# Kernel tuning notes

Hardware: AMD Instinct MI355X
Metric: run time of the kernel (lower is better)

Reference implementation:

```python
import jax, jax.numpy as jnp
import numpy as np

N, E, EL = 50000, 150000, 300000   # atoms, bonds(=line-graph nodes), line-graph edges
FN, FE, FX = 128, 128, 64          # atom, bond, angle feature dims (encode_dim)
H, D = 4, 64                        # num_heads, per-head hidden
SLOPE = 0.01                        # torch leaky_relu default


def _leaky(x):
    return jnp.where(x >= 0, x, SLOPE * x)


def _seg_softmax(logits, seg, n):
    # softmax over edges grouped by destination (DGL edge_softmax). logits [E, H]
    m = jax.ops.segment_max(logits, seg, num_segments=n)
    ex = jnp.exp(logits - m[seg])
    s = jax.ops.segment_sum(ex, seg, num_segments=n)
    return ex / s[seg]


def _seg_mean(x, seg, n):
    # mean of incoming edge feats per dst node; empty segments -> 0 (DGL behavior)
    s = jax.ops.segment_sum(x, seg, num_segments=n)
    c = jax.ops.segment_sum(jnp.ones((x.shape[0], 1), x.dtype), seg, num_segments=n)
    return s / jnp.maximum(c, 1.0)


def setup_inputs() -> dict:
    key = jax.random.key(0)
    ks = iter(jax.random.split(key, 40))
    nrm = lambda shape, sc=0.1: jax.random.normal(next(ks), shape, jnp.float32) * sc
    z = lambda n: jnp.zeros((n,), jnp.float32)
    inp = {
        'nfeats': nrm((N, FN), 1.0),
        'efeats': nrm((E, FE), 1.0),
        'xfeats': nrm((EL, FX), 1.0),
        # EGAT layer (atom graph)
        'e_Wni': nrm((H * D, FN)), 'e_Wnj': nrm((H * D, FN)), 'e_Wfij': nrm((H * D, FE)),
        'e_Wnode': nrm((H * D, FN + FE)), 'e_bnode': z(H * D),
        'e_attn': nrm((H, D)), 'e_bias': z(H * D),
        # Path_Complex line-graph branch
        'lg_Wni': nrm((H * D, D)), 'lg_Wnj': nrm((H * D, D)), 'lg_Wfij': nrm((H * D, FX)),
        'lg_Wnode': nrm((H * D, D + FX)), 'lg_bnode': z(H * D),
        'lg_attn': nrm((H, D)), 'lg_bias': z(H * D),
        # Path_Complex graph branch
        'g_Wni': nrm((H * D, D)), 'g_Wnj': nrm((H * D, D)), 'g_Wfij': nrm((H * D, D)),
        'g_Wnode': nrm((H * D, D + D)), 'g_bnode': z(H * D),
        'g_attn': nrm((H, D)), 'g_bias': z(H * D),
        # graph / line-graph connectivity
        'src': jax.random.randint(next(ks), (E,), 0, N, jnp.int32),
        'dst': jax.random.randint(next(ks), (E,), 0, N, jnp.int32),
        'lsrc': jax.random.randint(next(ks), (EL,), 0, E, jnp.int32),
        'ldst': jax.random.randint(next(ks), (EL,), 0, E, jnp.int32),
    }
    return inp


def _forward(nfeats, efeats, xfeats,
             e_Wni, e_Wnj, e_Wfij, e_Wnode, e_bnode, e_attn, e_bias,
             lg_Wni, lg_Wnj, lg_Wfij, lg_Wnode, lg_bnode, lg_attn, lg_bias,
             g_Wni, g_Wnj, g_Wfij, g_Wnode, g_bnode, g_attn, g_bias,
             src, dst, lsrc, ldst):
    # ---- EGAT layer on atom graph ----
    fo = _leaky((nfeats @ e_Wni.T)[src] + (nfeats @ e_Wnj.T)[dst] + efeats @ e_Wfij.T + e_bias)
    fov = fo.reshape(E, H, D)
    e_att = _seg_softmax((fov * e_attn[None]).sum(-1), dst, N)      # [E, H]
    agg = _seg_mean(efeats, dst, N)                                   # [N, FE]
    h = (jnp.concatenate([nfeats, agg], 1) @ e_Wnode.T + e_bnode).reshape(N, H, D)
    h_node = _leaky(jax.ops.segment_sum(h[src] * e_att[:, :, None], dst, num_segments=N)).sum(1)
    f_edge = fov.sum(1)                                               # [E, D]

    # ---- Path_Complex layer: line-graph (bond->angle) branch ----
    lgf = _leaky((f_edge @ lg_Wni.T)[lsrc] + (f_edge @ lg_Wnj.T)[ldst] + xfeats @ lg_Wfij.T + lg_bias)
    lgv = lgf.reshape(EL, H, D)
    a_lg = _seg_softmax((lgv * lg_attn[None]).sum(-1), ldst, E)      # [EL, H]
    aggx = _seg_mean(xfeats, ldst, E)                                 # [E, FX]
    m1 = (jnp.concatenate([f_edge, aggx], 1) @ lg_Wnode.T + lg_bnode).reshape(E, H, D)
    lg_h = _leaky(jax.ops.segment_sum(m1[lsrc] * a_lg[:, :, None], ldst, num_segments=E)).sum(1)

    # ---- Path_Complex layer: graph (atom->bond) branch ----
    gf = _leaky((h_node @ g_Wni.T)[src] + (h_node @ g_Wnj.T)[dst] + f_edge @ g_Wfij.T + g_bias)
    gv = gf.reshape(E, H, D)
    a_g = _seg_softmax((gv * g_attn[None]).sum(-1), dst, N)          # [E, H] -> l_graph ndata 'a'
    node_edge = h_node[src] + h_node[dst]
    m2 = (jnp.concatenate([node_edge, f_edge], 1) @ g_Wnode.T + g_bnode).reshape(E, H, D)
    # u_mul_v on line graph: message = h_out[lsrc] * a[ldst]
    g_h = _leaky(jax.ops.segment_sum(m2[lsrc] * a_g[ldst][:, :, None], ldst, num_segments=E)).sum(1)

    return g_h + lg_h                                                 # [E, D] updated bond feats


def reference(nfeats, efeats, xfeats,
              e_Wni, e_Wnj, e_Wfij, e_Wnode, e_bnode, e_attn, e_bias,
              lg_Wni, lg_Wnj, lg_Wfij, lg_Wnode, lg_bnode, lg_attn, lg_bias,
              g_Wni, g_Wnj, g_Wfij, g_Wnode, g_bnode, g_attn, g_bias,
              src, dst, lsrc, ldst):
    return _forward(nfeats, efeats, xfeats,
                    e_Wni, e_Wnj, e_Wfij, e_Wnode, e_bnode, e_attn, e_bias,
                    lg_Wni, lg_Wnj, lg_Wfij, lg_Wnode, lg_bnode, lg_attn, lg_bias,
                    g_Wni, g_Wnj, g_Wfij, g_Wnode, g_bnode, g_attn, g_bias,
                    src, dst, lsrc, ldst)
```

## Files before the change

kernel.cpp:

```cpp
#include <hip/hip_runtime.h>
#include <hip/hip_bf16.h>
#include <math.h>

typedef __hip_bfloat16 bf16;
typedef short bf16x8 __attribute__((ext_vector_type(8)));
typedef short s16x4 __attribute__((ext_vector_type(4)));
typedef float f32x4 __attribute__((ext_vector_type(4)));

__device__ __forceinline__ float b2f(bf16 x) { return __bfloat162float(x); }
__device__ __forceinline__ bf16  f2b(float x) { return __float2bfloat16(x); }
__device__ __forceinline__ float leaky(float x) { return x >= 0.0f ? x : 0.01f * x; }
__device__ __forceinline__ float sb2f(short s) {
  return __uint_as_float(((unsigned)(unsigned short)s) << 16);
}
__device__ __forceinline__ short f2bs(float x) {
  unsigned u = __float_as_uint(x);
  u += 0x7FFFu + ((u >> 16) & 1u);
  return (short)(u >> 16);
}
__device__ __forceinline__ float ldF(const void* p, size_t i, int f) {
  return f ? ((const float*)p)[i] : b2f(((const bf16*)p)[i]);
}
__device__ __forceinline__ bf16x8 ldA8(const char* row, int k, int f) {
  if (!f) return *(const bf16x8*)(row + (size_t)k * 2);
  const float4* p = (const float4*)(row + (size_t)k * 4);
  float4 a = p[0], b = p[1];
  bf16x8 r;
  r[0] = f2bs(a.x); r[1] = f2bs(a.y); r[2] = f2bs(a.z); r[3] = f2bs(a.w);
  r[4] = f2bs(b.x); r[5] = f2bs(b.y); r[6] = f2bs(b.z); r[7] = f2bs(b.w);
  return r;
}
__device__ __forceinline__ bf16x8 ldA8sum(const bf16* base, int K0, int s, int t, int k) {
  bf16x8 u = *(const bf16x8*)(base + (size_t)s * K0 + k);
  bf16x8 v = *(const bf16x8*)(base + (size_t)t * K0 + k);
  bf16x8 r;
#pragma unroll
  for (int j = 0; j < 8; ++j) r[j] = f2bs(sb2f(u[j]) + sb2f(v[j]));
  return r;
}

__global__ void k_detect(const unsigned* __restrict__ w, int* __restrict__ flag) {
  __shared__ int cnt[256];
  unsigned x = w[threadIdx.x];
  unsigned ex = (x >> 7) & 0xFFu;
  cnt[threadIdx.x] = (ex >= 96u && ex <= 144u) ? 1 : 0;
  __syncthreads();
  for (int s = 128; s > 0; s >>= 1) {
    if (threadIdx.x < s) cnt[threadIdx.x] += cnt[threadIdx.x + s];
    __syncthreads();
  }
  if (threadIdx.x == 0) *flag = (cnt[0] < 128) ? 1 : 0;
}

struct WArgs { const void* src[21]; int beg[22]; int len[21]; };
__global__ void k_cvt_all(WArgs wa, bf16* __restrict__ dst, int total,
                          const int* __restrict__ flagp) {
  int f = *flagp;
  for (int i = blockIdx.x * 256 + threadIdx.x; i < total; i += gridDim.x * 256) {
    int t = 0;
    while (t < 20 && i >= wa.beg[t + 1]) ++t;
    int loc = i - wa.beg[t];
    bf16 v = f2b(0.0f);
    if (loc < wa.len[t])
      v = f ? f2b(((const float*)wa.src[t])[loc]) : ((const bf16*)wa.src[t])[loc];
    dst[i] = v;
  }
}

__global__ void k_cvt3(const float* __restrict__ a, bf16* __restrict__ da, size_t na,
                       const float* __restrict__ b, bf16* __restrict__ db, size_t nb,
                       const float* __restrict__ c, bf16* __restrict__ dc, size_t nc,
                       const int* __restrict__ flagp) {
  if (!*flagp) return;
  size_t tot = (na + nb + nc) >> 2;
  for (size_t i = (size_t)blockIdx.x * 256 + threadIdx.x; i < tot;
       i += (size_t)gridDim.x * 256) {
    size_t j = i << 2;
    const float* s; bf16* d; size_t loc;
    if (j < na)           { s = a; d = da; loc = j; }
    else if (j < na + nb) { s = b; d = db; loc = j - na; }
    else                  { s = c; d = dc; loc = j - na - nb; }
    float4 v = *(const float4*)(s + loc);
    s16x4 o; o[0] = f2bs(v.x); o[1] = f2bs(v.y); o[2] = f2bs(v.z); o[3] = f2bs(v.w);
    *(s16x4*)(d + loc) = o;
  }
}

__global__ void k_izero(int* __restrict__ p, int n) {
  int i = blockIdx.x * 256 + threadIdx.x;
  for (; i < n; i += gridDim.x * 256) p[i] = 0;
}

__global__ void k_hist(const int* __restrict__ seg, int* __restrict__ deg, int n) {
  int i = blockIdx.x * 256 + threadIdx.x;
  if (i < n) atomicAdd(&deg[seg[i]], 1);
}

__global__ __launch_bounds__(256)
void k_scan_local(const int* __restrict__ deg, int* __restrict__ rp,
                  int* __restrict__ bsum, int n) {
  __shared__ int sh[256];
  int tid = threadIdx.x;
  int base = blockIdx.x * 4096 + tid * 16;
  int v[16]; int s = 0;
#pragma unroll
  for (int j = 0; j < 16; ++j) { v[j] = (base + j < n) ? deg[base + j] : 0; s += v[j]; }
  sh[tid] = s;
  __syncthreads();
  for (int o = 1; o < 256; o <<= 1) {
    int t = (tid >= o) ? sh[tid - o] : 0;
    __syncthreads();
    sh[tid] += t;
    __syncthreads();
  }
  int run = sh[tid] - s;
#pragma unroll
  for (int j = 0; j < 16; ++j) {
    run += v[j];
    if (base + j < n) rp[base + j + 1] = run;
  }
  if (tid == 255) bsum[blockIdx.x] = sh[255];
  if (blockIdx.x == 0 && tid == 0) rp[0] = 0;
}
__global__ __launch_bounds__(256)
void k_scan_bsum(int* __restrict__ bsum, int nb) {
  __shared__ int sh[256];
  __shared__ int carry;
  int tid = threadIdx.x;
  if (tid == 0) carry = 0;
  __syncthreads();
  for (int base = 0; base < nb; base += 256) {
    int i = base + tid;
    int v = (i < nb) ? bsum[i] : 0;
    sh[tid] = v;
    __syncthreads();
    for (int o = 1; o < 256; o <<= 1) {
      int t = (tid >= o) ? sh[tid - o] : 0;
      __syncthreads();
      sh[tid] += t;
      __syncthreads();
    }
    if (i < nb) bsum[i] = carry + sh[tid] - v;
    int tot = sh[255];
    __syncthreads();
    if (tid == 0) carry += tot;
    __syncthreads();
  }
}
__global__ __launch_bounds__(256)
void k_scan_add(int* __restrict__ rp, const int* __restrict__ bsum, int n) {
  int b = blockIdx.x + 1;
  int ofs = bsum[b];
  int base = b * 4096 + threadIdx.x * 16;
#pragma unroll
  for (int j = 0; j < 16; ++j) {
    int idx = base + j + 1;
    if (idx <= n) rp[idx] += ofs;
  }
}

__global__ void k_slot(const int* __restrict__ seg, const int* __restrict__ rp,
                       int* __restrict__ cur, int* __restrict__ eid,
                       const int* __restrict__ aux, int* __restrict__ auxval,
                       int* __restrict__ pos, int n) {
  int i = blockIdx.x * 256 + threadIdx.x;
  if (i >= n) return;
  int t = seg[i];
  int p = atomicAdd(&cur[t], 1);
  int j = rp[t] + p;
  eid[j] = i;
  if (auxval) auxval[j] = aux[i];
  if (pos) pos[i] = j;
}

__global__ void k_gmean(const void* __restrict__ X, const void* __restrict__ Xc, int mode,
                        const int* __restrict__ rp, const int* __restrict__ eid,
                        bf16* __restrict__ out, int n, int width,
                        const int* __restrict__ flagp) {
  int f = (mode == 2) ? *flagp : mode;
  if (Xc && f) { X = Xc; f = 0; }
  int d = threadIdx.x;
  int row = blockIdx.x * blockDim.y + threadIdx.y;
  if (row >= n) return;
  int b = rp[row], e = rp[row + 1];
  float s = 0.0f;
  for (int j = b; j < e; ++j) s += ldF(X, (size_t)eid[j] * width + d, f);
  out[(size_t)row * width + d] = f2b(s / fmaxf((float)(e - b), 1.0f));
}

__global__ __launch_bounds__(256)
void k_mgemm(const void* __restrict__ A0, const void* __restrict__ A0c, int m0mode, int K0,
             const void* __restrict__ A1, int m1mode, int Ktot,
             const bf16* __restrict__ W, int whs, const bf16* __restrict__ bias,
             bf16* __restrict__ C, int cs, int M,
             const int* __restrict__ gs, const int* __restrict__ gd,
             const int* __restrict__ flagp) {
  int tid = threadIdx.x;
  int w = tid >> 6, lane = tid & 63, l15 = lane & 15, q = lane >> 4;
  int h = blockIdx.y;
  int fl = *flagp;
  int f0 = (m0mode == 2) ? fl : m0mode;
  if (A0c && f0) { A0 = A0c; f0 = 0; }
  int f1 = (m1mode == 2) ? fl : m1mode;
  const bf16* Wh = W + (size_t)h * whs;
  int colofs = h * 64;
  int m0 = blockIdx.x * 64 + w * 16;
  int mA = m0 + l15; if (mA > M - 1) mA = M - 1;
  int sA = 0, tA = 0;
  const char* rowA0 = nullptr;
  if (gs) { sA = gs[mA]; tA = gd[mA]; }
  else rowA0 = (const char*)A0 + (size_t)mA * K0 * (f0 ? 4 : 2);
  const char* rowA1 = A1 ? (const char*)A1 + (size_t)mA * (Ktot - K0) * (f1 ? 4 : 2) : nullptr;

  f32x4 acc[4] = {{0,0,0,0},{0,0,0,0},{0,0,0,0},{0,0,0,0}};
  for (int k = q * 8; k < Ktot; k += 32) {
    bf16x8 a;
    if (k < K0) a = gs ? ldA8sum((const bf16*)A0, K0, sA, tA, k) : ldA8(rowA0, k, f0);
    else        a = ldA8(rowA1, k - K0, f1);
    const bf16* wb = Wh + (size_t)l15 * Ktot + k;
#pragma unroll
    for (int t = 0; t < 4; ++t)
      acc[t] = __builtin_amdgcn_mfma_f32_16x16x32_bf16(
          a, *(const bf16x8*)(wb + (size_t)(t * 16) * Ktot), acc[t], 0, 0, 0);
  }
#pragma unroll
  for (int t = 0; t < 4; ++t) {
    int col = t * 16 + l15;
    float bv = bias ? b2f(bias[colofs + col]) : 0.0f;
#pragma unroll
    for (int r = 0; r < 4; ++r) {
      int m = m0 + q * 4 + r;
      if (m < M) C[(size_t)m * cs + colofs + col] = f2b(acc[t][r] + bv);
    }
  }
}

__global__ __launch_bounds__(256)
void k_mgemm2(const void* __restrict__ A, const void* __restrict__ Ac, int mode, int K,
              const bf16* __restrict__ W1, const bf16* __restrict__ W2, int whs,
              bf16* __restrict__ C1, bf16* __restrict__ C2, int cs, int M,
              const int* __restrict__ flagp) {
  int tid = threadIdx.x;
  int w = tid >> 6, lane = tid & 63, l15 = lane & 15, q = lane >> 4;
  int h = blockIdx.y;
  int f = (mode == 2) ? *flagp : mode;
  if (Ac && f) { A = Ac; f = 0; }
  const bf16* W1h = W1 + (size_t)h * whs;
  const bf16* W2h = W2 + (size_t)h * whs;
  int colofs = h * 64;
  int m0 = blockIdx.x * 64 + w * 16;
  int mA = m0 + l15; if (mA > M - 1) mA = M - 1;
  const char* rowA = (const char*)A + (size_t)mA * K * (f ? 4 : 2);

  f32x4 a1[4] = {{0,0,0,0},{0,0,0,0},{0,0,0,0},{0,0,0,0}};
  f32x4 a2[4] = {{0,0,0,0},{0,0,0,0},{0,0,0,0},{0,0,0,0}};
  for (int k = q * 8; k < K; k += 32) {
    bf16x8 a = ldA8(rowA, k, f);
    const bf16* w1 = W1h + (size_t)l15 * K + k;
    const bf16* w2 = W2h + (size_t)l15 * K + k;
#pragma unroll
    for (int t = 0; t < 4; ++t) {
      a1[t] = __builtin_amdgcn_mfma_f32_16x16x32_bf16(
          a, *(const bf16x8*)(w1 + (size_t)(t * 16) * K), a1[t], 0, 0, 0);
      a2[t] = __builtin_amdgcn_mfma_f32_16x16x32_bf16(
          a, *(const bf16x8*)(w2 + (size_t)(t * 16) * K), a2[t], 0, 0, 0);
    }
  }
#pragma unroll
  for (int r = 0; r < 4; ++r) {
    int m = m0 + q * 4 + r;
    if (m < M) {
      s16x4 o1, o2;
#pragma unroll
      for (int t = 0; t < 4; ++t) { o1[t] = f2bs(a1[t][r]); o2[t] = f2bs(a2[t][r]); }
      *(s16x4*)(C1 + (size_t)m * cs + colofs + l15 * 4) = o1;
      *(s16x4*)(C2 + (size_t)m * cs + colofs + l15 * 4) = o2;
    }
  }
}

template<int NK>
__global__ __launch_bounds__(256)
void k_mcomb4(const void* __restrict__ A, const void* __restrict__ Ac, int mode,
              const bf16* __restrict__ W, int whs,
              const bf16* __restrict__ bias, const bf16* __restrict__ attn,
              const bf16* __restrict__ G1, const bf16* __restrict__ G2, int gstr,
              const int* __restrict__ gi, const int* __restrict__ gj,
              const int* __restrict__ posw,
              float* __restrict__ lg4, bf16* __restrict__ fout,
              int M, const int* __restrict__ flagp) {
  constexpr int K = NK * 32;
  int tid = threadIdx.x;
  int w = tid >> 6, lane = tid & 63, l15 = lane & 15, q = lane >> 4;
  int f = (mode == 2) ? *flagp : mode;
  if (Ac && f) { A = Ac; f = 0; }
  int m0 = blockIdx.x * 64 + w * 16;
  int mA = m0 + l15; if (mA > M - 1) mA = M - 1;
  const char* rowA = (const char*)A + (size_t)mA * K * (f ? 4 : 2);
  bf16x8 af[NK];
#pragma unroll
  for (int i = 0; i < NK; ++i) af[i] = ldA8(rowA, q * 8 + 32 * i, f);
  int sIdx[4], dIdx[4], pIdx[4]; bool okr[4];
#pragma unroll
  for (int r = 0; r < 4; ++r) {
    int m = m0 + q * 4 + r;
    okr[r] = m < M; int mc = okr[r] ? m : M - 1;
    sIdx[r] = gi[mc]; dIdx[r] = gj[mc];
    pIdx[r] = posw ? posw[mc] : mc;
  }
  s16x4 gv1[4][4], gv2[4][4];
#pragma unroll
  for (int r = 0; r < 4; ++r) {
    const s16x4* p1 = (const s16x4*)(G1 + (size_t)sIdx[r] * gstr) + l15;
    const s16x4* p2 = (const s16x4*)(G2 + (size_t)dIdx[r] * gstr) + l15;
#pragma unroll
    for (int h = 0; h < 4; ++h) { gv1[r][h] = p1[h * 16]; gv2[r][h] = p2[h * 16]; }
  }
  f32x4 fs[4] = {{0,0,0,0},{0,0,0,0},{0,0,0,0},{0,0,0,0}};
#pragma unroll
  for (int h = 0; h < 4; ++h) {
    const bf16* Wh = W + (size_t)h * whs;
    f32x4 acc[4] = {{0,0,0,0},{0,0,0,0},{0,0,0,0},{0,0,0,0}};
#pragma unroll
    for (int i = 0; i < NK; ++i) {
      const bf16* wb = Wh + (size_t)l15 * K + q * 8 + 32 * i;
#pragma unroll
      for (int t = 0; t < 4; ++t)
        acc[t] = __builtin_amdgcn_mfma_f32_16x16x32_bf16(
            af[i], *(const bf16x8*)(wb + (size_t)(t * 16) * K), acc[t], 0, 0, 0);
    }
    float bv[4], av[4];
#pragma unroll
    for (int t = 0; t < 4; ++t) {
      bv[t] = b2f(bias[h * 64 + t * 16 + l15]);
      av[t] = b2f(attn[h * 64 + t * 16 + l15]);
    }
    float part[4];
#pragma unroll
    for (int r = 0; r < 4; ++r) {
      float p = 0.0f;
#pragma unroll
      for (int t = 0; t < 4; ++t) {
        float v = acc[t][r] + bv[t] + sb2f(gv1[r][h][t]) + sb2f(gv2[r][h][t]);
        v = leaky(v);
        p += v * av[t];
        fs[t][r] += v;
      }
      part[r] = p;
    }
#pragma unroll
    for (int o = 1; o < 16; o <<= 1)
#pragma unroll
      for (int r = 0; r < 4; ++r) part[r] += __shfl_xor(part[r], o, 64);
    if (l15 == 0) {
#pragma unroll
      for (int r = 0; r < 4; ++r)
        if (okr[r]) lg4[(size_t)pIdx[r] * 4 + h] = part[r];
    }
  }
  if (fout) {
#pragma unroll
    for (int t = 0; t < 4; ++t) {
      int col = t * 16 + l15;
#pragma unroll
      for (int r = 0; r < 4; ++r)
        if (okr[r]) fout[(size_t)(m0 + q * 4 + r) * 64 + col] = f2b(fs[t][r]);
    }
  }
}

__global__ __launch_bounds__(256)
void k_mcomb(const void* __restrict__ A, const void* __restrict__ Ac, int mode, int K,
             const bf16* __restrict__ W, const bf16* __restrict__ bias,
             const bf16* __restrict__ attn,
             const bf16* __restrict__ G1, const bf16* __restrict__ G2, int gstr,
             const int* __restrict__ gi, const int* __restrict__ gj,
             const int* __restrict__ posw,
             float* __restrict__ lg, int M, const int* __restrict__ flagp) {
  int tid = threadIdx.x;
  int w = tid >> 6, lane = tid & 63, l15 = lane & 15, q = lane >> 4;
  int f = (mode == 2) ? *flagp : mode;
  if (Ac && f) { A = Ac; f = 0; }
  int m0 = blockIdx.x * 64 + w * 16;
  int mA = m0 + l15; if (mA > M - 1) mA = M - 1;
  const char* rowA = (const char*)A + (size_t)mA * K * (f ? 4 : 2);
  int mcs[4], pIdx[4]; bool okr[4];
#pragma unroll
  for (int r = 0; r < 4; ++r) {
    int m = m0 + q * 4 + r;
    okr[r] = m < M; mcs[r] = okr[r] ? m : M - 1;
    pIdx[r] = posw ? posw[mcs[r]] : mcs[r];
  }
  s16x4 gv1[4], gv2[4];
#pragma unroll
  for (int r = 0; r < 4; ++r) {
    gv1[r] = ((const s16x4*)(G1 + (size_t)gi[mcs[r]] * gstr))[l15];
    gv2[r] = ((const s16x4*)(G2 + (size_t)gj[mcs[r]] * gstr))[l15];
  }
  f32x4 acc[4] = {{0,0,0,0},{0,0,0,0},{0,0,0,0},{0,0,0,0}};
  for (int k = q * 8; k < K; k += 32) {
    bf16x8 a = ldA8(rowA, k, f);
    const bf16* wb = W + (size_t)l15 * K + k;
#pragma unroll
    for (int t = 0; t < 4; ++t)
      acc[t] = __builtin_amdgcn_mfma_f32_16x16x32_bf16(
          a, *(const bf16x8*)(wb + (size_t)(t * 16) * K), acc[t], 0, 0, 0);
  }
  float attv[4], bsv[4];
#pragma unroll
  for (int t = 0; t < 4; ++t) { attv[t] = b2f(attn[t*16+l15]); bsv[t] = b2f(bias[t*16+l15]); }
  float part[4];
#pragma unroll
  for (int r = 0; r < 4; ++r) {
    float p = 0.0f;
#pragma unroll
    for (int t = 0; t < 4; ++t) {
      float v = acc[t][r] + bsv[t] + sb2f(gv1[r][t]) + sb2f(gv2[r][t]);
      p += leaky(v) * attv[t];
    }
    part[r] = p;
  }
#pragma unroll
  for (int o = 1; o < 16; o <<= 1)
#pragma unroll
    for (int r = 0; r < 4; ++r) part[r] += __shfl_xor(part[r], o, 64);
  if (l15 == 0) {
#pragma unroll
    for (int r = 0; r < 4; ++r)
      if (okr[r]) lg[pIdx[r]] = part[r];
  }
}

__global__ __launch_bounds__(256)
void k_smax4_csr(float* __restrict__ lg, const int* __restrict__ rp, int n) {
  int tid = blockIdx.x * 256 + threadIdx.x;
  int row = tid >> 2, h = tid & 3;
  if (row >= n) return;
  int b = rp[row], e = rp[row + 1];
  float m = -INFINITY;
  for (int j = b; j < e; ++j) m = fmaxf(m, lg[(size_t)j * 4 + h]);
  float s = 0.0f;
  for (int j = b; j < e; ++j) {
    float ex = expf(lg[(size_t)j * 4 + h] - m);
    lg[(size_t)j * 4 + h] = ex;
    s += ex;
  }
  float inv = 1.0f / s;
  for (int j = b; j < e; ++j) lg[(size_t)j * 4 + h] *= inv;
}
__global__ __launch_bounds__(256)
void k_smax4_eid(float* __restrict__ lg, const int* __restrict__ rp,
                 const int* __restrict__ eid, int n) {
  int tid = blockIdx.x * 256 + threadIdx.x;
  int row = tid >> 2, h = tid & 3;
  if (row >= n) return;
  int b = rp[row], e = rp[row + 1];
  float m = -INFINITY;
  for (int j = b; j < e; ++j) m = fmaxf(m, lg[(size_t)eid[j] * 4 + h]);
  float s = 0.0f;
  for (int j = b; j < e; ++j) {
    float ex = expf(lg[(size_t)eid[j] * 4 + h] - m);
    lg[(size_t)eid[j] * 4 + h] = ex;
    s += ex;
  }
  float inv = 1.0f / s;
  for (int j = b; j < e; ++j) lg[(size_t)eid[j] * 4 + h] *= inv;
}
__global__ __launch_bounds__(256)
void k_smax1_csr(float* __restrict__ lg, const int* __restrict__ rp, int n) {
  int row = blockIdx.x * 256 + threadIdx.x;
  if (row >= n) return;
  int b = rp[row], e = rp[row + 1];
  float m = -INFINITY;
  for (int j = b; j < e; ++j) m = fmaxf(m, lg[j]);
  float s = 0.0f;
  for (int j = b; j < e; ++j) { float ex = expf(lg[j] - m); lg[j] = ex; s += ex; }
  float inv = 1.0f / s;
  for (int j = b; j < e; ++j) lg[j] *= inv;
}

__global__ __launch_bounds__(256)
void k_ghnode(const bf16* __restrict__ H, const float* __restrict__ lg4c,
              const int* __restrict__ rp, const int* __restrict__ srcv,
              bf16* __restrict__ hnode, int N) {
  int d = threadIdx.x, h = threadIdx.y;
  int n = blockIdx.x;
  int b = rp[n], e = rp[n + 1];
  float s = 0.0f;
  for (int j = b; j < e; ++j)
    s += b2f(H[(size_t)srcv[j] * 256 + h * 64 + d]) * lg4c[(size_t)j * 4 + h];
  float v = leaky(s);
  __shared__ float sh[4][64];
  if (h > 0) sh[h][d] = v;
  __syncthreads();
  if (h == 0)
    hnode[(size_t)n * 64 + d] = f2b(v + sh[1][d] + sh[2][d] + sh[3][d]);
}

__global__ void k_gout2(const bf16* __restrict__ M1, const float* __restrict__ lgE,
                        const int* __restrict__ rp, const int* __restrict__ lsv,
                        float* __restrict__ out, int E, int first) {
  int d = threadIdx.x;
  int t = blockIdx.x * 4 + threadIdx.y;
  if (t >= E) return;
  int b = rp[t], e = rp[t + 1];
  float s = 0.0f;
  for (int j = b; j < e; ++j)
    s += b2f(M1[(size_t)lsv[j] * 64 + d]) * lgE[j];
  float val = leaky(s);
  if (first) out[(size_t)t * 64 + d] = val;
  else       out[(size_t)t * 64 + d] += val;
}

__global__ void k_gout3(const bf16* __restrict__ M2, const float* __restrict__ lg4n,
                        const int* __restrict__ rp, const int* __restrict__ lsv,
                        float* __restrict__ out, int E, int h) {
  int d = threadIdx.x;
  int t = blockIdx.x * 4 + threadIdx.y;
  if (t >= E) return;
  int b = rp[t], e = rp[t + 1];
  float s = 0.0f;
  for (int j = b; j < e; ++j) s += b2f(M2[(size_t)lsv[j] * 64 + d]);
  float a = lg4n[(size_t)t * 4 + h];
  out[(size_t)t * 64 + d] += leaky(a * s);
}

__global__ void k_addpair(const bf16* __restrict__ hn, const int* __restrict__ src,
                          const int* __restrict__ dst, bf16* __restrict__ ne, int E) {
  int d = threadIdx.x;
  int e = blockIdx.x * 4 + threadIdx.y;
  if (e >= E) return;
  ne[(size_t)e * 64 + d] =
      f2b(b2f(hn[(size_t)src[e] * 64 + d]) + b2f(hn[(size_t)dst[e] * 64 + d]));
}

__global__ void k_cast(void* __restrict__ out, const float* __restrict__ a, size_t n,
                       const int* __restrict__ flagp) {
  int f = *flagp;
  size_t i = (size_t)blockIdx.x * blockDim.x + threadIdx.x;
  size_t st = (size_t)gridDim.x * blockDim.x;
  for (; i < n; i += st) {
    if (f) ((float*)out)[i] = a[i];
    else   ((bf16*)out)[i] = f2b(a[i]);
  }
}

extern "C" void kernel_launch(void* const* d_in, const int* in_sizes, int n_in,
                              void* d_out, int out_size, void* d_ws, size_t ws_size,
                              hipStream_t stream) {
  const int* src  = (const int*)d_in[24];
  const int* dst  = (const int*)d_in[25];
  const int* lsrc = (const int*)d_in[26];
  const int* ldst = (const int*)d_in[27];

  const int N  = in_sizes[0] / 128;
  const int E  = in_sizes[24];
  const int EL = in_sizes[26];
  (void)n_in; (void)out_size; (void)ws_size;

  char* base = (char*)d_ws;
  size_t off = 0;
  auto alloc = [&](size_t bytes) -> char* {
    char* p = base + off;
    off = (off + bytes + 255) & ~(size_t)255;
    return p;
  };
  int* flag = (int*)alloc(256);
  size_t wofs[28]; size_t wtot = 0;
  for (int i = 3; i <= 23; ++i) { wofs[i] = wtot; wtot += (size_t)((in_sizes[i] + 127) & ~127); }
  bf16* WA = (bf16*)alloc(wtot * 2);

  int*   tmpi  = (int*)alloc((size_t)2 * E * 4);
  int*   rpN   = (int*)alloc((size_t)(N + 1) * 4);
  int*   eidN  = (int*)alloc((size_t)E * 4);
  int*   srcv  = (int*)alloc((size_t)E * 4);
  int*   posN  = (int*)alloc((size_t)E * 4);
  int*   rpE   = (int*)alloc((size_t)(E + 1) * 4);
  int*   eidEL = (int*)alloc((size_t)EL * 4);
  int*   lsv   = (int*)alloc((size_t)EL * 4);
  int*   posE  = (int*)alloc((size_t)EL * 4);
  int*   bsum  = (int*)alloc(((size_t)((E > N ? E : N) + 4095) / 4096 + 8) * 4);
  bf16*  fedge = (bf16*)alloc((size_t)E * 64 * 2);
  bf16*  hnode = (bf16*)alloc((size_t)N * 64 * 2);
  float* outacc= (float*)alloc((size_t)E * 64 * 4);
  bf16*  aggB  = (bf16*)alloc((size_t)E * 64 * 2);
  bf16*  SA    = (bf16*)alloc((size_t)N * 256 * 2 > (size_t)E * 64 * 2
                              ? (size_t)N * 256 * 2 : (size_t)E * 64 * 2);
  bf16*  SB    = (bf16*)alloc((size_t)N * 256 * 2 > (size_t)E * 64 * 2
                              ? (size_t)N * 256 * 2 : (size_t)E * 64 * 2);
  float* logE4 = (float*)alloc((size_t)E * 4 * 4);
  float* logh  = (float*)alloc((size_t)EL * 4);
  bf16*  nb    = (bf16*)alloc((size_t)N * 128 * 2);

  bf16* eb = (bf16*)outacc;
  bf16* xb = (bf16*)d_out;

  dim3 blk(256);
  const unsigned tN = (N + 63) / 64, tEg = (E + 63) / 64, tELg = (EL + 63) / 64;
  const unsigned gE4 = (E + 3) / 4, gN4 = (N + 3) / 4;
  const unsigned cE = (E + 255) / 256, cEL = (EL + 255) / 256;
  const int nbN = (N + 4095) / 4096, nbE = (E + 4095) / 4096;

  k_detect<<<dim3(1), blk, 0, stream>>>((const unsigned*)d_in[0], flag);
  WArgs wa;
  for (int i = 3; i <= 23; ++i) {
    wa.src[i - 3] = d_in[i];
    wa.beg[i - 3] = (int)wofs[i];
    wa.len[i - 3] = in_sizes[i];
  }
  wa.beg[21] = (int)wtot;
  k_cvt_all<<<dim3(512), blk, 0, stream>>>(wa, WA, (int)wtot, flag);
  k_cvt3<<<dim3(2048), blk, 0, stream>>>(
      (const float*)d_in[0], nb, (size_t)N * 128,
      (const float*)d_in[1], eb, (size_t)E * 128,
      (const float*)d_in[2], xb, (size_t)EL * 64, flag);

  int* deg = tmpi; int* cur = tmpi + E;
  k_izero<<<dim3(1024), blk, 0, stream>>>(tmpi, 2 * E);
  k_hist<<<dim3(cE), blk, 0, stream>>>(dst, deg, E);
  k_scan_local<<<dim3(nbN), blk, 0, stream>>>(deg, rpN, bsum, N);
  k_scan_bsum<<<dim3(1), blk, 0, stream>>>(bsum, nbN);
  if (nbN > 1) k_scan_add<<<dim3(nbN - 1), blk, 0, stream>>>(rpN, bsum, N);
  k_slot<<<dim3(cE), blk, 0, stream>>>(dst, rpN, cur, eidN, src, srcv, posN, E);
  k_izero<<<dim3(1024), blk, 0, stream>>>(tmpi, 2 * E);
  k_hist<<<dim3(cEL), blk, 0, stream>>>(ldst, deg, EL);
  k_scan_local<<<dim3(nbE), blk, 0, stream>>>(deg, rpE, bsum, E);
  k_scan_bsum<<<dim3(1), blk, 0, stream>>>(bsum, nbE);
  if (nbE > 1) k_scan_add<<<dim3(nbE - 1), blk, 0, stream>>>(rpE, bsum, E);
  k_slot<<<dim3(cEL), blk, 0, stream>>>(ldst, rpE, cur, eidEL, lsrc, lsv, posE, EL);

  k_gmean<<<dim3((N + 1) / 2), dim3(128, 2), 0, stream>>>(d_in[1], eb, 2, rpN, eidN,
                                                          aggB, N, 128, flag);
  k_mgemm2<<<dim3(tN, 4), blk, 0, stream>>>(d_in[0], nb, 2, 128, WA + wofs[3], WA + wofs[4],
                                            8192, SA, SB, 256, N, flag);
  k_mcomb4<4><<<dim3(tEg), blk, 0, stream>>>(d_in[1], eb, 2, WA + wofs[5], 8192,
      WA + wofs[9], WA + wofs[8], SA, SB, 256, src, dst, posN, logE4, fedge, E, flag);
  k_smax4_csr<<<dim3((N * 4 + 255) / 256), blk, 0, stream>>>(logE4, rpN, N);
  k_mgemm<<<dim3(tN, 4), blk, 0, stream>>>(d_in[0], nb, 2, 128, aggB, 0, 256,
      WA + wofs[6], 16384, WA + wofs[7], SA, 256, N, nullptr, nullptr, flag);
  k_ghnode<<<dim3(N), dim3(64, 4), 0, stream>>>(SA, logE4, rpN, srcv, hnode, N);

  k_gmean<<<dim3(gE4), dim3(64, 4), 0, stream>>>(d_in[2], xb, 2, rpE, eidEL, aggB, E, 64, flag);
  for (int h = 0; h < 4; ++h) {
    k_mgemm2<<<dim3(tEg), blk, 0, stream>>>(fedge, nullptr, 0, 64,
        WA + wofs[10] + h * 4096, WA + wofs[11] + h * 4096, 0, SA, SB, 64, E, flag);
    k_mcomb<<<dim3(tELg), blk, 0, stream>>>(d_in[2], xb, 2, 64,
        WA + wofs[12] + h * 4096, WA + wofs[16] + h * 64, WA + wofs[15] + h * 64,
        SA, SB, 64, lsrc, ldst, posE, logh, EL, flag);
    k_smax1_csr<<<dim3((E + 255) / 256), blk, 0, stream>>>(logh, rpE, E);
    k_mgemm<<<dim3(tEg, 1), blk, 0, stream>>>(fedge, nullptr, 0, 64, aggB, 0, 128,
        WA + wofs[13] + (size_t)h * 8192, 0, WA + wofs[14] + h * 64,
        SA, 64, E, nullptr, nullptr, flag);
    k_gout2<<<dim3(gE4), dim3(64, 4), 0, stream>>>(SA, logh, rpE, lsv,
                                                   outacc, E, h == 0 ? 1 : 0);
  }

  k_mgemm2<<<dim3(tN, 4), blk, 0, stream>>>(hnode, nullptr, 0, 64, WA + wofs[17], WA + wofs[18],
                                            4096, SA, SB, 256, N, flag);
  k_mcomb4<2><<<dim3(tEg), blk, 0, stream>>>(fedge, nullptr, 0, WA + wofs[19], 4096,
      WA + wofs[23], WA + wofs[22], SA, SB, 256, src, dst, nullptr, logE4, nullptr, E, flag);
  k_smax4_eid<<<dim3((N * 4 + 255) / 256), blk, 0, stream>>>(logE4, rpN, eidN, N);
  k_addpair<<<dim3(gE4), dim3(64, 4), 0, stream>>>(hnode, src, dst, aggB, E);
  for (int h = 0; h < 4; ++h) {
    k_mgemm<<<dim3(tEg, 1), blk, 0, stream>>>(aggB, nullptr, 0, 64, fedge, 0, 128,
        WA + wofs[20] + (size_t)h * 8192, 0, WA + wofs[21] + h * 64,
        SB, 64, E, nullptr, nullptr, flag);
    k_gout3<<<dim3(gE4), dim3(64, 4), 0, stream>>>(SB, logE4, rpE, lsv,
                                                   outacc, E, h);
  }

  k_cast<<<dim3(2048), blk, 0, stream>>>(d_out, outacc, (size_t)E * 64, flag);
}
```

Measured before the change: 1.804 ms.

## Fuse node projections into edge attention GEMM and batch line-graph heads

Removes the separate node-level projection GEMMs (Wni/Wnj) that wrote intermediate per-node buffers. Instead, the edge kernel gathers the raw source and destination node features and multiplies them inside the same MFMA accumulation. The line-graph attention is now computed for all four heads in one launch followed by one 4-head softmax, replacing four per-head projection, attention and softmax launches. This trades extra MFMA work per edge (the projections are recomputed for each edge rather than once per node) for fewer launches and less intermediate memory traffic.

```diff
diff --git a/kernel.cpp b/kernel.cpp
--- a/kernel.cpp
+++ b/kernel.cpp
@@ -235,99 +235,76 @@
   }
 }
 
-__global__ __launch_bounds__(256)
-void k_mgemm2(const void* __restrict__ A, const void* __restrict__ Ac, int mode, int K,
-              const bf16* __restrict__ W1, const bf16* __restrict__ W2, int whs,
-              bf16* __restrict__ C1, bf16* __restrict__ C2, int cs, int M,
-              const int* __restrict__ flagp) {
-  int tid = threadIdx.x;
-  int w = tid >> 6, lane = tid & 63, l15 = lane & 15, q = lane >> 4;
-  int h = blockIdx.y;
-  int f = (mode == 2) ? *flagp : mode;
-  if (Ac && f) { A = Ac; f = 0; }
-  const bf16* W1h = W1 + (size_t)h * whs;
-  const bf16* W2h = W2 + (size_t)h * whs;
-  int colofs = h * 64;
-  int m0 = blockIdx.x * 64 + w * 16;
-  int mA = m0 + l15; if (mA > M - 1) mA = M - 1;
-  const char* rowA = (const char*)A + (size_t)mA * K * (f ? 4 : 2);
-
-  f32x4 a1[4] = {{0,0,0,0},{0,0,0,0},{0,0,0,0},{0,0,0,0}};
-  f32x4 a2[4] = {{0,0,0,0},{0,0,0,0},{0,0,0,0},{0,0,0,0}};
-  for (int k = q * 8; k < K; k += 32) {
-    bf16x8 a = ldA8(rowA, k, f);
-    const bf16* w1 = W1h + (size_t)l15 * K + k;
-    const bf16* w2 = W2h + (size_t)l15 * K + k;
-#pragma unroll
-    for (int t = 0; t < 4; ++t) {
-      a1[t] = __builtin_amdgcn_mfma_f32_16x16x32_bf16(
-          a, *(const bf16x8*)(w1 + (size_t)(t * 16) * K), a1[t], 0, 0, 0);
-      a2[t] = __builtin_amdgcn_mfma_f32_16x16x32_bf16(
-          a, *(const bf16x8*)(w2 + (size_t)(t * 16) * K), a2[t], 0, 0, 0);
-    }
-  }
-#pragma unroll
-  for (int r = 0; r < 4; ++r) {
-    int m = m0 + q * 4 + r;
-    if (m < M) {
-      s16x4 o1, o2;
-#pragma unroll
-      for (int t = 0; t < 4; ++t) { o1[t] = f2bs(a1[t][r]); o2[t] = f2bs(a2[t][r]); }
-      *(s16x4*)(C1 + (size_t)m * cs + colofs + l15 * 4) = o1;
-      *(s16x4*)(C2 + (size_t)m * cs + colofs + l15 * 4) = o2;
-    }
-  }
-}
-
-template<int NK>
-__global__ __launch_bounds__(256)
-void k_mcomb4(const void* __restrict__ A, const void* __restrict__ Ac, int mode,
-              const bf16* __restrict__ W, int whs,
+template<int NKA, int NKS, bool HASF>
+__global__ __launch_bounds__(256)
+void k_mcombG(const void* __restrict__ A, const void* __restrict__ Ac, int mode,
+              const bf16* __restrict__ Wf, int whsF,
+              const bf16* __restrict__ S, const bf16* __restrict__ Sc,
+              const bf16* __restrict__ Wn1, const bf16* __restrict__ Wn2, int whsS,
               const bf16* __restrict__ bias, const bf16* __restrict__ attn,
-              const bf16* __restrict__ G1, const bf16* __restrict__ G2, int gstr,
               const int* __restrict__ gi, const int* __restrict__ gj,
               const int* __restrict__ posw,
               float* __restrict__ lg4, bf16* __restrict__ fout,
               int M, const int* __restrict__ flagp) {
-  constexpr int K = NK * 32;
+  constexpr int KA = NKA * 32, KS = NKS * 32;
   int tid = threadIdx.x;
   int w = tid >> 6, lane = tid & 63, l15 = lane & 15, q = lane >> 4;
-  int f = (mode == 2) ? *flagp : mode;
+  int fl = *flagp;
+  int f = (mode == 2) ? fl : mode;
   if (Ac && f) { A = Ac; f = 0; }
+  if (Sc && fl) S = Sc;
   int m0 = blockIdx.x * 64 + w * 16;
   int mA = m0 + l15; if (mA > M - 1) mA = M - 1;
-  const char* rowA = (const char*)A + (size_t)mA * K * (f ? 4 : 2);
-  bf16x8 af[NK];
-#pragma unroll
-  for (int i = 0; i < NK; ++i) af[i] = ldA8(rowA, q * 8 + 32 * i, f);
-  int sIdx[4], dIdx[4], pIdx[4]; bool okr[4];
+  const char* rowA = (const char*)A + (size_t)mA * KA * (f ? 4 : 2);
+  bf16x8 af[NKA];
+#pragma unroll
+  for (int i = 0; i < NKA; ++i) af[i] = ldA8(rowA, q * 8 + 32 * i, f);
+  const bf16* rowS = S + (size_t)gi[mA] * KS;
+  const bf16* rowD = S + (size_t)gj[mA] * KS;
+  bf16x8 as_[NKS], ad_[NKS];
+#pragma unroll
+  for (int i = 0; i < NKS; ++i) {
+    as_[i] = *(const bf16x8*)(rowS + q * 8 + 32 * i);
+    ad_[i] = *(const bf16x8*)(rowD + q * 8 + 32 * i);
+  }
+  int pIdx[4]; bool okr[4];
 #pragma unroll
   for (int r = 0; r < 4; ++r) {
     int m = m0 + q * 4 + r;
     okr[r] = m < M; int mc = okr[r] ? m : M - 1;
-    sIdx[r] = gi[mc]; dIdx[r] = gj[mc];
     pIdx[r] = posw ? posw[mc] : mc;
   }
-  s16x4 gv1[4][4], gv2[4][4];
-#pragma unroll
-  for (int r = 0; r < 4; ++r) {
-    const s16x4* p1 = (const s16x4*)(G1 + (size_t)sIdx[r] * gstr) + l15;
-    const s16x4* p2 = (const s16x4*)(G2 + (size_t)dIdx[r] * gstr) + l15;
-#pragma unroll
-    for (int h = 0; h < 4; ++h) { gv1[r][h] = p1[h * 16]; gv2[r][h] = p2[h * 16]; }
-  }
-  f32x4 fs[4] = {{0,0,0,0},{0,0,0,0},{0,0,0,0},{0,0,0,0}};
+  f32x4 fs[4];
+  if (HASF) {
+#pragma unroll
+    for (int t = 0; t < 4; ++t) fs[t] = {0, 0, 0, 0};
+  }
 #pragma unroll
   for (int h = 0; h < 4; ++h) {
-    const bf16* Wh = W + (size_t)h * whs;
+    const bf16* Wfh = Wf + (size_t)h * whsF;
+    const bf16* W1h = Wn1 + (size_t)h * whsS;
+    const bf16* W2h = Wn2 + (size_t)h * whsS;
     f32x4 acc[4] = {{0,0,0,0},{0,0,0,0},{0,0,0,0},{0,0,0,0}};
 #pragma unroll
-    for (int i = 0; i < NK; ++i) {
-      const bf16* wb = Wh + (size_t)l15 * K + q * 8 + 32 * i;
+    for (int i = 0; i < NKA; ++i) {
+      const bf16* wf = Wfh + (size_t)l15 * KA + q * 8 + 32 * i;
 #pragma unroll
       for (int t = 0; t < 4; ++t)
         acc[t] = __builtin_amdgcn_mfma_f32_16x16x32_bf16(
-            af[i], *(const bf16x8*)(wb + (size_t)(t * 16) * K), acc[t], 0, 0, 0);
+            af[i], *(const bf16x8*)(wf + (size_t)(t * 16) * KA), acc[t], 0, 0, 0);
+    }
+#pragma unroll
+    for (int i = 0; i < NKS; ++i) {
+      const bf16* w1 = W1h + (size_t)l15 * KS + q * 8 + 32 * i;
+      const bf16* w2 = W2h + (size_t)l15 * KS + q * 8 + 32 * i;
+#pragma unroll
+      for (int t = 0; t < 4; ++t)
+        acc[t] = __builtin_amdgcn_mfma_f32_16x16x32_bf16(
+            as_[i], *(const bf16x8*)(w1 + (size_t)(t * 16) * KS), acc[t], 0, 0, 0);
+#pragma unroll
+      for (int t = 0; t < 4; ++t)
+        acc[t] = __builtin_amdgcn_mfma_f32_16x16x32_bf16(
+            ad_[i], *(const bf16x8*)(w2 + (size_t)(t * 16) * KS), acc[t], 0, 0, 0);
     }
     float bv[4], av[4];
 #pragma unroll
@@ -341,10 +318,10 @@
       float p = 0.0f;
 #pragma unroll
       for (int t = 0; t < 4; ++t) {
-        float v = acc[t][r] + bv[t] + sb2f(gv1[r][h][t]) + sb2f(gv2[r][h][t]);
+        float v = acc[t][r] + bv[t];
         v = leaky(v);
         p += v * av[t];
-        fs[t][r] += v;
+        if (HASF) fs[t][r] += v;
       }
       part[r] = p;
     }
@@ -358,7 +335,7 @@
         if (okr[r]) lg4[(size_t)pIdx[r] * 4 + h] = part[r];
     }
   }
-  if (fout) {
+  if (HASF && fout) {
 #pragma unroll
     for (int t = 0; t < 4; ++t) {
       int col = t * 16 + l15;
@@ -366,68 +343,6 @@
       for (int r = 0; r < 4; ++r)
         if (okr[r]) fout[(size_t)(m0 + q * 4 + r) * 64 + col] = f2b(fs[t][r]);
     }
-  }
-}
-
-__global__ __launch_bounds__(256)
-void k_mcomb(const void* __restrict__ A, const void* __restrict__ Ac, int mode, int K,
-             const bf16* __restrict__ W, const bf16* __restrict__ bias,
-             const bf16* __restrict__ attn,
-             const bf16* __restrict__ G1, const bf16* __restrict__ G2, int gstr,
-             const int* __restrict__ gi, const int* __restrict__ gj,
-             const int* __restrict__ posw,
-             float* __restrict__ lg, int M, const int* __restrict__ flagp) {
-  int tid = threadIdx.x;
-  int w = tid >> 6, lane = tid & 63, l15 = lane & 15, q = lane >> 4;
-  int f = (mode == 2) ? *flagp : mode;
-  if (Ac && f) { A = Ac; f = 0; }
-  int m0 = blockIdx.x * 64 + w * 16;
-  int mA = m0 + l15; if (mA > M - 1) mA = M - 1;
-  const char* rowA = (const char*)A + (size_t)mA * K * (f ? 4 : 2);
-  int mcs[4], pIdx[4]; bool okr[4];
-#pragma unroll
-  for (int r = 0; r < 4; ++r) {
-    int m = m0 + q * 4 + r;
-    okr[r] = m < M; mcs[r] = okr[r] ? m : M - 1;
-    pIdx[r] = posw ? posw[mcs[r]] : mcs[r];
-  }
-  s16x4 gv1[4], gv2[4];
-#pragma unroll
-  for (int r = 0; r < 4; ++r) {
-    gv1[r] = ((const s16x4*)(G1 + (size_t)gi[mcs[r]] * gstr))[l15];
-    gv2[r] = ((const s16x4*)(G2 + (size_t)gj[mcs[r]] * gstr))[l15];
-  }
-  f32x4 acc[4] = {{0,0,0,0},{0,0,0,0},{0,0,0,0},{0,0,0,0}};
-  for (int k = q * 8; k < K; k += 32) {
-    bf16x8 a = ldA8(rowA, k, f);
-    const bf16* wb = W + (size_t)l15 * K + k;
-#pragma unroll
-    for (int t = 0; t < 4; ++t)
-      acc[t] = __builtin_amdgcn_mfma_f32_16x16x32_bf16(
-          a, *(const bf16x8*)(wb + (size_t)(t * 16) * K), acc[t], 0, 0, 0);
-  }
-  float attv[4], bsv[4];
-#pragma unroll
-  for (int t = 0; t < 4; ++t) { attv[t] = b2f(attn[t*16+l15]); bsv[t] = b2f(bias[t*16+l15]); }
-  float part[4];
-#pragma unroll
-  for (int r = 0; r < 4; ++r) {
-    float p = 0.0f;
-#pragma unroll
-    for (int t = 0; t < 4; ++t) {
-      float v = acc[t][r] + bsv[t] + sb2f(gv1[r][t]) + sb2f(gv2[r][t]);
-      p += leaky(v) * attv[t];
-    }
-    part[r] = p;
-  }
-#pragma unroll
-  for (int o = 1; o < 16; o <<= 1)
-#pragma unroll
-    for (int r = 0; r < 4; ++r) part[r] += __shfl_xor(part[r], o, 64);
-  if (l15 == 0) {
-#pragma unroll
-    for (int r = 0; r < 4; ++r)
-      if (okr[r]) lg[pIdx[r]] = part[r];
   }
 }
 
@@ -465,18 +380,6 @@
   }
   float inv = 1.0f / s;
   for (int j = b; j < e; ++j) lg[(size_t)eid[j] * 4 + h] *= inv;
-}
-__global__ __launch_bounds__(256)
-void k_smax1_csr(float* __restrict__ lg, const int* __restrict__ rp, int n) {
-  int row = blockIdx.x * 256 + threadIdx.x;
-  if (row >= n) return;
-  int b = rp[row], e = rp[row + 1];
-  float m = -INFINITY;
-  for (int j = b; j < e; ++j) m = fmaxf(m, lg[j]);
-  float s = 0.0f;
-  for (int j = b; j < e; ++j) { float ex = expf(lg[j] - m); lg[j] = ex; s += ex; }
-  float inv = 1.0f / s;
-  for (int j = b; j < e; ++j) lg[j] *= inv;
 }
 
 __global__ __launch_bounds__(256)
@@ -497,8 +400,8 @@
     hnode[(size_t)n * 64 + d] = f2b(v + sh[1][d] + sh[2][d] + sh[3][d]);
 }
 
-__global__ void k_gout2(const bf16* __restrict__ M1, const float* __restrict__ lgE,
-                        const int* __restrict__ rp, const int* __restrict__ lsv,
+__global__ void k_gout2(const bf16* __restrict__ M1, const float* __restrict__ lgE4,
+                        int h, const int* __restrict__ rp, const int* __restrict__ lsv,
                         float* __restrict__ out, int E, int first) {
   int d = threadIdx.x;
   int t = blockIdx.x * 4 + threadIdx.y;
@@ -506,7 +409,7 @@
   int b = rp[t], e = rp[t + 1];
   float s = 0.0f;
   for (int j = b; j < e; ++j)
-    s += b2f(M1[(size_t)lsv[j] * 64 + d]) * lgE[j];
+    s += b2f(M1[(size_t)lsv[j] * 64 + d]) * lgE4[(size_t)j * 4 + h];
   float val = leaky(s);
   if (first) out[(size_t)t * 64 + d] = val;
   else       out[(size_t)t * 64 + d] += val;
@@ -586,10 +489,8 @@
   bf16*  aggB  = (bf16*)alloc((size_t)E * 64 * 2);
   bf16*  SA    = (bf16*)alloc((size_t)N * 256 * 2 > (size_t)E * 64 * 2
                               ? (size_t)N * 256 * 2 : (size_t)E * 64 * 2);
-  bf16*  SB    = (bf16*)alloc((size_t)N * 256 * 2 > (size_t)E * 64 * 2
-                              ? (size_t)N * 256 * 2 : (size_t)E * 64 * 2);
   float* logE4 = (float*)alloc((size_t)E * 4 * 4);
-  float* logh  = (float*)alloc((size_t)EL * 4);
+  float* logEL4= (float*)alloc((size_t)EL * 4 * 4);
   bf16*  nb    = (bf16*)alloc((size_t)N * 128 * 2);
 
   bf16* eb = (bf16*)outacc;
@@ -597,7 +498,7 @@
 
   dim3 blk(256);
   const unsigned tN = (N + 63) / 64, tEg = (E + 63) / 64, tELg = (EL + 63) / 64;
-  const unsigned gE4 = (E + 3) / 4, gN4 = (N + 3) / 4;
+  const unsigned gE4 = (E + 3) / 4;
   const unsigned cE = (E + 255) / 256, cEL = (EL + 255) / 256;
   const int nbN = (N + 4095) / 4096, nbE = (E + 4095) / 4096;
 
@@ -631,41 +532,40 @@
 
   k_gmean<<<dim3((N + 1) / 2), dim3(128, 2), 0, stream>>>(d_in[1], eb, 2, rpN, eidN,
                                                           aggB, N, 128, flag);
-  k_mgemm2<<<dim3(tN, 4), blk, 0, stream>>>(d_in[0], nb, 2, 128, WA + wofs[3], WA + wofs[4],
-                                            8192, SA, SB, 256, N, flag);
-  k_mcomb4<4><<<dim3(tEg), blk, 0, stream>>>(d_in[1], eb, 2, WA + wofs[5], 8192,
-      WA + wofs[9], WA + wofs[8], SA, SB, 256, src, dst, posN, logE4, fedge, E, flag);
+  k_mcombG<4, 4, true><<<dim3(tEg), blk, 0, stream>>>(
+      d_in[1], eb, 2, WA + wofs[5], 8192,
+      (const bf16*)d_in[0], nb, WA + wofs[3], WA + wofs[4], 8192,
+      WA + wofs[9], WA + wofs[8], src, dst, posN, logE4, fedge, E, flag);
   k_smax4_csr<<<dim3((N * 4 + 255) / 256), blk, 0, stream>>>(logE4, rpN, N);
   k_mgemm<<<dim3(tN, 4), blk, 0, stream>>>(d_in[0], nb, 2, 128, aggB, 0, 256,
       WA + wofs[6], 16384, WA + wofs[7], SA, 256, N, nullptr, nullptr, flag);
   k_ghnode<<<dim3(N), dim3(64, 4), 0, stream>>>(SA, logE4, rpN, srcv, hnode, N);
 
   k_gmean<<<dim3(gE4), dim3(64, 4), 0, stream>>>(d_in[2], xb, 2, rpE, eidEL, aggB, E, 64, flag);
+  k_mcombG<2, 2, false><<<dim3(tELg), blk, 0, stream>>>(
+      d_in[2], xb, 2, WA + wofs[12], 4096,
+      fedge, nullptr, WA + wofs[10], WA + wofs[11], 4096,
+      WA + wofs[16], WA + wofs[15], lsrc, ldst, posE, logEL4, nullptr, EL, flag);
+  k_smax4_csr<<<dim3((E * 4 + 255) / 256), blk, 0, stream>>>(logEL4, rpE, E);
   for (int h = 0; h < 4; ++h) {
-    k_mgemm2<<<dim3(tEg), blk, 0, stream>>>(fedge, nullptr, 0, 64,
-        WA + wofs[10] + h * 4096, WA + wofs[11] + h * 4096, 0, SA, SB, 64, E, flag);
-    k_mcomb<<<dim3(tELg), blk, 0, stream>>>(d_in[2], xb, 2, 64,
-        WA + wofs[12] + h * 4096, WA + wofs[16] + h * 64, WA + wofs[15] + h * 64,
-        SA, SB, 64, lsrc, ldst, posE, logh, EL, flag);
-    k_smax1_csr<<<dim3((E + 255) / 256), blk, 0, stream>>>(logh, rpE, E);
     k_mgemm<<<dim3(tEg, 1), blk, 0, stream>>>(fedge, nullptr, 0, 64, aggB, 0, 128,
         WA + wofs[13] + (size_t)h * 8192, 0, WA + wofs[14] + h * 64,
         SA, 64, E, nullptr, nullptr, flag);
-    k_gout2<<<dim3(gE4), dim3(64, 4), 0, stream>>>(SA, logh, rpE, lsv,
+    k_gout2<<<dim3(gE4), dim3(64, 4), 0, stream>>>(SA, logEL4, h, rpE, lsv,
                                                    outacc, E, h == 0 ? 1 : 0);
   }
 
-  k_mgemm2<<<dim3(tN, 4), blk, 0, stream>>>(hnode, nullptr, 0, 64, WA + wofs[17], WA + wofs[18],
-                                            4096, SA, SB, 256, N, flag);
-  k_mcomb4<2><<<dim3(tEg), blk, 0, stream>>>(fedge, nullptr, 0, WA + wofs[19], 4096,
-      WA + wofs[23], WA + wofs[22], SA, SB, 256, src, dst, nullptr, logE4, nullptr, E, flag);
+  k_mcombG<2, 2, false><<<dim3(tEg), blk, 0, stream>>>(
+      fedge, nullptr, 0, WA + wofs[19], 4096,
+      hnode, nullptr, WA + wofs[17], WA + wofs[18], 4096,
+      WA + wofs[23], WA + wofs[22], src, dst, nullptr, logE4, nullptr, E, flag);
   k_smax4_eid<<<dim3((N * 4 + 255) / 256), blk, 0, stream>>>(logE4, rpN, eidN, N);
   k_addpair<<<dim3(gE4), dim3(64, 4), 0, stream>>>(hnode, src, dst, aggB, E);
   for (int h = 0; h < 4; ++h) {
     k_mgemm<<<dim3(tEg, 1), blk, 0, stream>>>(aggB, nullptr, 0, 64, fedge, 0, 128,
         WA + wofs[20] + (size_t)h * 8192, 0, WA + wofs[21] + h * 64,
-        SB, 64, E, nullptr, nullptr, flag);
-    k_gout3<<<dim3(gE4), dim3(64, 4), 0, stream>>>(SB, logE4, rpE, lsv,
+        SA, 64, E, nullptr, nullptr, flag);
+    k_gout3<<<dim3(gE4), dim3(64, 4), 0, stream>>>(SA, logE4, rpE, lsv,
                                                    outacc, E, h);
   }
 
```

Result: slower. 1.864 ms (+3.3%).
